# Kernel optimization log

Measured on AMD Instinct MI355X. Metric: run time of the kernel, lower is better.

Reference implementation:

```python
import jax, jax.numpy as jnp
import numpy as np

N = 50000        # nodes
E = 1600000      # edges (before self loops)
D_IN = 768       # roberta-base hidden size
SIZES = [256, 256]
NEG_SLOPE = 0.2
EPS = 1e-16


def setup_inputs() -> dict:
    key = jax.random.key(0)
    ks = jax.random.split(key, 16)
    s = 0.05
    inp = {
        "x": jax.random.normal(ks[0], (N, D_IN), dtype=jnp.float32),
        "edge_index": jax.random.randint(ks[1], (2, E), 0, N, dtype=jnp.int64),
        # GAT layer 0
        "W0": jax.random.normal(ks[2], (D_IN, SIZES[0]), dtype=jnp.float32) * s,
        "a_src0": jax.random.normal(ks[3], (SIZES[0],), dtype=jnp.float32) * s,
        "a_dst0": jax.random.normal(ks[4], (SIZES[0],), dtype=jnp.float32) * s,
        "b0": jnp.zeros((SIZES[0],), dtype=jnp.float32),
        # GAT layer 1
        "W1": jax.random.normal(ks[5], (SIZES[0], SIZES[1]), dtype=jnp.float32) * s,
        "a_src1": jax.random.normal(ks[6], (SIZES[1],), dtype=jnp.float32) * s,
        "a_dst1": jax.random.normal(ks[7], (SIZES[1],), dtype=jnp.float32) * s,
        "b1": jnp.zeros((SIZES[1],), dtype=jnp.float32),
        # GlobalAttention gate_nn: Linear(256 -> 1)
        "gate_w": jax.random.normal(ks[8], (SIZES[1], 1), dtype=jnp.float32) * s,
        "gate_b": jnp.zeros((1,), dtype=jnp.float32),
    }
    return inp


def _gat_layer(x, src, dst, W, a_src, a_dst, b):
    # PyG GATConv, heads=1: h = x W; e_ij = leaky_relu(a_src.h_j + a_dst.h_i)
    # softmax over edges grouped by target node i, then weighted aggregation.
    h = x @ W                                   # [N, D]
    alpha_src = h @ a_src                       # [N]
    alpha_dst = h @ a_dst                       # [N]
    e = jax.nn.leaky_relu(alpha_src[src] + alpha_dst[dst], NEG_SLOPE)  # [E']
    e_max = jax.ops.segment_max(e, dst, num_segments=N)
    e = jnp.exp(e - e_max[dst])
    denom = jax.ops.segment_sum(e, dst, num_segments=N)
    alpha = e / (denom[dst] + EPS)              # [E'] softmax per target
    out = jax.ops.segment_sum(alpha[:, None] * h[src], dst, num_segments=N)
    return out + b


def reference(x, edge_index, W0, a_src0, a_dst0, b0, W1, a_src1, a_dst1, b1, gate_w, gate_b):
    # add self loops (GATConv default add_self_loops=True)
    loop = jnp.arange(N, dtype=edge_index.dtype)
    src = jnp.concatenate([edge_index[0], loop])
    dst = jnp.concatenate([edge_index[1], loop])

    h = jax.nn.relu(_gat_layer(x, src, dst, W0, a_src0, a_dst0, b0))
    h = jax.nn.relu(_gat_layer(h, src, dst, W1, a_src1, a_dst1, b1))

    # GlobalAttention pooling over the single graph
    gate = h @ gate_w + gate_b                  # [N, 1]
    attn = jax.nn.softmax(gate, axis=0)         # softmax over nodes
    out = jnp.sum(attn * h, axis=0, keepdims=True)  # [1, 256]
    return out
```

## Files before the change

kernel.cpp:

```cpp
#include <hip/hip_runtime.h>

typedef unsigned int uint;
typedef unsigned short u16;
typedef unsigned char u8;

typedef __attribute__((ext_vector_type(8))) short short8;
typedef __attribute__((ext_vector_type(8))) u16 u16x8;
typedef __attribute__((ext_vector_type(4))) float f32x4;
typedef __attribute__((ext_vector_type(2))) float f32x2;

#define NN 50000
#define EE 1600000
#define ETOT (EE + NN)
#define NBUCK 782
#define ACHUNK 8192
#define CAP 2432
#define NSLOT 64
#define SLOTW 260

__device__ __forceinline__ u16 f2bf(float f) {
  uint u = __builtin_bit_cast(uint, f);
  uint r = u + 0x7fffu + ((u >> 16) & 1u);
  return (u16)(r >> 16);
}
__device__ __forceinline__ float bf2f(u16 h) {
  return __builtin_bit_cast(float, ((uint)h) << 16);
}
__device__ __forceinline__ u8 f2fp8(float f) {
  int t = __builtin_amdgcn_cvt_pk_fp8_f32(f, f, 0, false);
  return (u8)(t & 0xff);
}
__device__ __forceinline__ float wred_sum(float v) {
#pragma unroll
  for (int off = 32; off > 0; off >>= 1) v += __shfl_xor(v, off);
  return v;
}

__global__ void zero_ws(uint* __restrict__ bnxt, float* __restrict__ slots) {
  int i = blockIdx.x * 256 + threadIdx.x;
  if (i < NBUCK) bnxt[i] = 0u;
  if (i < NSLOT * SLOTW) slots[i] = 0.f;
}

__global__ void wt_both(const float* __restrict__ W0, const float* __restrict__ W1,
                        u16* __restrict__ Wt0, u16* __restrict__ Wt1) {
  int i = blockIdx.x * 256 + threadIdx.x;
  if (i < 768 * 256) {
    int k = i >> 8, n = i & 255;
    Wt0[n * 768 + k] = f2bf(W0[i]);
  } else if (i < 768 * 256 + 256 * 256) {
    int j = i - 768 * 256;
    int k = j >> 8, n = j & 255;
    Wt1[n * 256 + k] = f2bf(W1[j]);
  }
}

template <bool ABF16>
__global__ __launch_bounds__(512) void gemm_fused(const void* __restrict__ Avoid,
                                                  const u16* __restrict__ Bt,
                                                  u8* __restrict__ C8,
                                                  const float* __restrict__ a_src,
                                                  const float* __restrict__ a_dst,
                                                  float* __restrict__ as_,
                                                  float* __restrict__ ad_,
                                                  int M, int K) {
  __shared__ __align__(16) u16 As[128 * 64];
  __shared__ __align__(16) u16 Bs[256 * 64];
  __shared__ float asLds[4][128];
  __shared__ float adLds[4][128];
  const int m0 = blockIdx.x * 128;
  const int tid = threadIdx.x;
  const int lane = tid & 63;
  const int wv = tid >> 6;
  const int wm = wv >> 2, wn = wv & 3;

  f32x4 acc[4][4] = {};

  const int sr = tid >> 2;
  const int skc = (tid & 3) * 16;
  const int br = tid >> 1;
  const int bk = (tid & 1) * 32;

  for (int k0 = 0; k0 < K; k0 += 64) {
    {
      int grow = m0 + sr;
      if constexpr (!ABF16) {
        const float* A = (const float*)Avoid;
        float4 f[4];
        if (grow < M) {
          const float4* src = reinterpret_cast<const float4*>(A + (size_t)grow * K + k0 + skc);
#pragma unroll
          for (int i = 0; i < 4; ++i) f[i] = src[i];
        } else {
#pragma unroll
          for (int i = 0; i < 4; ++i) f[i] = make_float4(0.f, 0.f, 0.f, 0.f);
        }
#pragma unroll
        for (int i = 0; i < 2; ++i) {
          u16x8 v;
          v[0] = f2bf(f[2 * i].x); v[1] = f2bf(f[2 * i].y);
          v[2] = f2bf(f[2 * i].z); v[3] = f2bf(f[2 * i].w);
          v[4] = f2bf(f[2 * i + 1].x); v[5] = f2bf(f[2 * i + 1].y);
          v[6] = f2bf(f[2 * i + 1].z); v[7] = f2bf(f[2 * i + 1].w);
          int k = skc + i * 8;
          int idx = (sr << 6) + (k ^ ((sr & 7) << 3));
          *reinterpret_cast<u16x8*>(&As[idx]) = v;
        }
      } else {
        const u16* A = (const u16*)Avoid;
        u16x8 v[2];
        if (grow < M) {
          const u16x8* src = reinterpret_cast<const u16x8*>(A + (size_t)grow * K + k0 + skc);
          v[0] = src[0]; v[1] = src[1];
        } else {
          v[0] = (u16x8)0; v[1] = (u16x8)0;
        }
#pragma unroll
        for (int i = 0; i < 2; ++i) {
          int k = skc + i * 8;
          int idx = (sr << 6) + (k ^ ((sr & 7) << 3));
          *reinterpret_cast<u16x8*>(&As[idx]) = v[i];
        }
      }
    }
    {
      const u16x8* src = reinterpret_cast<const u16x8*>(Bt + (size_t)br * K + k0 + bk);
#pragma unroll
      for (int i = 0; i < 4; ++i) {
        u16x8 v = src[i];
        int k = bk + i * 8;
        int idx = (br << 6) + (k ^ ((br & 7) << 3));
        *reinterpret_cast<u16x8*>(&Bs[idx]) = v;
      }
    }
    __syncthreads();
#pragma unroll
    for (int kk = 0; kk < 2; ++kk) {
      short8 af[4], bfr[4];
      const int kb = kk * 32 + (lane >> 4) * 8;
#pragma unroll
      for (int m = 0; m < 4; ++m) {
        int r = wm * 64 + m * 16 + (lane & 15);
        int idx = (r << 6) + (kb ^ ((r & 7) << 3));
        af[m] = *reinterpret_cast<const short8*>(&As[idx]);
      }
#pragma unroll
      for (int n = 0; n < 4; ++n) {
        int c = wn * 64 + n * 16 + (lane & 15);
        int idx = (c << 6) + (kb ^ ((c & 7) << 3));
        bfr[n] = *reinterpret_cast<const short8*>(&Bs[idx]);
      }
#pragma unroll
      for (int m = 0; m < 4; ++m)
#pragma unroll
        for (int n = 0; n < 4; ++n)
          acc[m][n] = __builtin_amdgcn_mfma_f32_16x16x32_bf16(af[m], bfr[n], acc[m][n], 0, 0, 0);
    }
    __syncthreads();
  }

  const int g = lane >> 4;
  const int cl = lane & 15;
  float asv[4], adv[4];
#pragma unroll
  for (int n = 0; n < 4; ++n) {
    int c = wn * 64 + n * 16 + cl;
    asv[n] = a_src[c];
    adv[n] = a_dst[c];
  }
#pragma unroll
  for (int m = 0; m < 4; ++m) {
#pragma unroll
    for (int reg = 0; reg < 4; ++reg) {
      int rl = wm * 64 + m * 16 + g * 4 + reg;
      int row = m0 + rl;
      float ps = 0.f, pd = 0.f;
      if (row < M) {
#pragma unroll
        for (int n = 0; n < 4; ++n) {
          float v = acc[m][n][reg];
          C8[(size_t)row * 256 + wn * 64 + n * 16 + cl] = f2fp8(v);
          ps = fmaf(v, asv[n], ps);
          pd = fmaf(v, adv[n], pd);
        }
      }
#pragma unroll
      for (int off = 1; off < 16; off <<= 1) {
        ps += __shfl_xor(ps, off);
        pd += __shfl_xor(pd, off);
      }
      if (cl == 0) {
        asLds[wn][rl] = ps;
        adLds[wn][rl] = pd;
      }
    }
  }
  __syncthreads();
  if (tid < 128) {
    int row = m0 + tid;
    if (row < M) {
      as_[row] = asLds[0][tid] + asLds[1][tid] + asLds[2][tid] + asLds[3][tid];
      ad_[row] = adLds[0][tid] + adLds[1][tid] + adLds[2][tid] + adLds[3][tid];
    }
  }
}

__global__ __launch_bounds__(256) void bucket_scatter(const int* __restrict__ esrc,
                                                      const int* __restrict__ edst,
                                                      uint* __restrict__ bnxt,
                                                      uint* __restrict__ tmp) {
  __shared__ uint lh[NBUCK];
  int base = blockIdx.x * ACHUNK;
  int nE = ETOT - base; if (nE > ACHUNK) nE = ACHUNK;
  for (int i = threadIdx.x; i < NBUCK; i += 256) lh[i] = 0;
  __syncthreads();
  for (int k = threadIdx.x; k < nE; k += 256) {
    int e = base + k;
    int d = (e < EE) ? edst[e] : (e - EE);
    atomicAdd(&lh[d >> 6], 1u);
  }
  __syncthreads();
  for (int i = threadIdx.x; i < NBUCK; i += 256) {
    uint c = lh[i];
    lh[i] = c ? atomicAdd(&bnxt[i], c) : 0u;
  }
  __syncthreads();
  for (int k = threadIdx.x; k < nE; k += 256) {
    int e = base + k;
    int s, d;
    if (e < EE) { s = esrc[e]; d = edst[e]; } else { s = e - EE; d = s; }
    uint pos = atomicAdd(&lh[d >> 6], 1u);
    tmp[(size_t)(d >> 6) * CAP + pos] = ((uint)(d & 63) << 16) | (uint)s;
  }
}

__global__ __launch_bounds__(1024) void scanb_kernel(const uint* __restrict__ bnxt,
                                                     uint* __restrict__ bptr) {
  __shared__ uint wsum[16];
  int tid = threadIdx.x, lane = tid & 63, w = tid >> 6;
  uint v = (tid < NBUCK) ? bnxt[tid] : 0u;
  uint x = v;
#pragma unroll
  for (int off = 1; off < 64; off <<= 1) {
    uint t = __shfl_up(x, off);
    if (lane >= off) x += t;
  }
  if (lane == 63) wsum[w] = x;
  __syncthreads();
  uint woff = 0;
  for (int k = 0; k < w; ++k) woff += wsum[k];
  uint excl = woff + x - v;
  if (tid < NBUCK) bptr[tid] = excl;
}

__global__ __launch_bounds__(256) void bucket_sort(const uint* __restrict__ tmp,
                                                   const uint* __restrict__ bptr,
                                                   const uint* __restrict__ bnxt,
                                                   uint* __restrict__ row_ptr,
                                                   u16* __restrict__ csr) {
  __shared__ uint lh[64];
  __shared__ uint buf[CAP];
  int b = blockIdx.x;
  uint s0 = bptr[b];
  int cnt = (int)bnxt[b];
  int tid = threadIdx.x;
  if (tid < 64) lh[tid] = 0;
  __syncthreads();
  for (int i = tid; i < cnt; i += 256) {
    uint v = tmp[(size_t)b * CAP + i];
    buf[i] = v;
    atomicAdd(&lh[v >> 16], 1u);
  }
  __syncthreads();
  if (tid < 64) {
    uint v = lh[tid];
    uint x = v;
#pragma unroll
    for (int off = 1; off < 64; off <<= 1) {
      uint t = __shfl_up(x, off);
      if (tid >= off) x += t;
    }
    uint pos = s0 + x - v;
    int d = b * 64 + tid;
    if (d < NN) row_ptr[d] = pos;
    lh[tid] = pos;
    if (b == NBUCK - 1 && tid == 0) row_ptr[NN] = s0 + (uint)cnt;
  }
  __syncthreads();
  for (int i = tid; i < cnt; i += 256) {
    uint v = buf[i];
    uint pos = atomicAdd(&lh[v >> 16], 1u);
    csr[pos] = (u16)(v & 0xFFFFu);
  }
}

template <bool POOL>
__global__ __launch_bounds__(256) void agg_kernel(const uint* __restrict__ h8,
                                                  const float* __restrict__ as_,
                                                  const float* __restrict__ ad_,
                                                  const uint* __restrict__ row_ptr,
                                                  const u16* __restrict__ csr_src,
                                                  const float* __restrict__ bias,
                                                  u16* __restrict__ out,
                                                  const float* __restrict__ gate_w,
                                                  float* __restrict__ slots, int n) {
  __shared__ float lp[257];
  int wid = (blockIdx.x * 256 + threadIdx.x) >> 6;
  int lane = threadIdx.x & 63;
  if (POOL) {
    for (int i = threadIdx.x; i < 257; i += 256) lp[i] = 0.f;
    __syncthreads();
  }
  if (wid < n) {
    uint start = row_ptr[wid], end = row_ptr[wid + 1];
    float adi = ad_[wid];
    float ax = 0.f, ay = 0.f, az = 0.f, aw = 0.f;
    float denom = 0.f;
    for (uint base = start; base < end; base += 64) {
      int cnt = (int)(end - base);
      if (cnt > 64) cnt = 64;
      float w = 0.f;
      int s = 0;
      if (lane < cnt) {
        s = (int)csr_src[base + lane];
        float e = as_[s] + adi;
        e = e > 0.f ? e : 0.2f * e;
        w = __expf(e);
      }
      denom += w;
      int j = 0;
      for (; j + 8 <= cnt; j += 8) {
        uint v[8];
        float ww[8];
#pragma unroll
        for (int q = 0; q < 8; ++q) {
          int sq = __shfl(s, j + q);
          ww[q] = __shfl(w, j + q);
          v[q] = h8[(size_t)sq * 64 + lane];
        }
#pragma unroll
        for (int q = 0; q < 8; ++q) {
          f32x2 lo = __builtin_amdgcn_cvt_pk_f32_fp8(v[q], false);
          f32x2 hi = __builtin_amdgcn_cvt_pk_f32_fp8(v[q], true);
          ax = fmaf(ww[q], lo.x, ax); ay = fmaf(ww[q], lo.y, ay);
          az = fmaf(ww[q], hi.x, az); aw = fmaf(ww[q], hi.y, aw);
        }
      }
      for (; j < cnt; ++j) {
        int sj = __shfl(s, j);
        float wj = __shfl(w, j);
        uint v = h8[(size_t)sj * 64 + lane];
        f32x2 lo = __builtin_amdgcn_cvt_pk_f32_fp8(v, false);
        f32x2 hi = __builtin_amdgcn_cvt_pk_f32_fp8(v, true);
        ax = fmaf(wj, lo.x, ax); ay = fmaf(wj, lo.y, ay);
        az = fmaf(wj, hi.x, az); aw = fmaf(wj, hi.y, aw);
      }
    }
    denom = wred_sum(denom);
    float inv = 1.f / (denom + 1e-16f);
    float4 b = reinterpret_cast<const float4*>(bias)[lane];
    float ox = fmaxf(fmaf(ax, inv, b.x), 0.f);
    float oy = fmaxf(fmaf(ay, inv, b.y), 0.f);
    float oz = fmaxf(fmaf(az, inv, b.z), 0.f);
    float ow = fmaxf(fmaf(aw, inv, b.w), 0.f);
    if (!POOL) {
      ushort4 o;
      o.x = f2bf(ox); o.y = f2bf(oy); o.z = f2bf(oz); o.w = f2bf(ow);
      reinterpret_cast<ushort4*>(out)[(size_t)wid * 64 + lane] = o;
    } else {
      float4 gv = reinterpret_cast<const float4*>(gate_w)[lane];
      float pg = wred_sum(ox * gv.x + oy * gv.y + oz * gv.z + ow * gv.w);
      float we = __expf(pg);
      int c0 = lane * 4;
      atomicAdd(&lp[c0 + 0], we * ox);
      atomicAdd(&lp[c0 + 1], we * oy);
      atomicAdd(&lp[c0 + 2], we * oz);
      atomicAdd(&lp[c0 + 3], we * ow);
      if (lane == 0) atomicAdd(&lp[256], we);
    }
  }
  if (POOL) {
    __syncthreads();
    int slot = blockIdx.x & (NSLOT - 1);
    for (int i = threadIdx.x; i < 257; i += 256) {
      float v = lp[i];
      if (v != 0.f) atomicAdd(&slots[slot * SLOTW + i], v);
    }
  }
}

__global__ void pool3_kernel(const float* __restrict__ slots, float* __restrict__ out) {
  __shared__ float dsh;
  int tid = threadIdx.x;
  float acc = 0.f;
  for (int s = 0; s < NSLOT; ++s) acc += slots[s * SLOTW + tid];
  if (tid == 0) {
    float d = 0.f;
    for (int s = 0; s < NSLOT; ++s) d += slots[s * SLOTW + 256];
    dsh = d;
  }
  __syncthreads();
  out[tid] = acc / dsh;
}

extern "C" void kernel_launch(void* const* d_in, const int* in_sizes, int n_in,
                              void* d_out, int out_size, void* d_ws, size_t ws_size,
                              hipStream_t stream) {
  const float* x = (const float*)d_in[0];
  const int* edge = (const int*)d_in[1];
  const float* W0 = (const float*)d_in[2];
  const float* a_src0 = (const float*)d_in[3];
  const float* a_dst0 = (const float*)d_in[4];
  const float* b0 = (const float*)d_in[5];
  const float* W1 = (const float*)d_in[6];
  const float* a_src1 = (const float*)d_in[7];
  const float* a_dst1 = (const float*)d_in[8];
  const float* b1 = (const float*)d_in[9];
  const float* gate_w = (const float*)d_in[10];
  float* out = (float*)d_out;

  char* p = (char*)d_ws;
  size_t off = 0;
  auto take = [&](size_t bytes) -> char* {
    char* r = p + off;
    off = (off + bytes + 255) & ~(size_t)255;
    return r;
  };
  u8* hA = (u8*)take((size_t)NN * 256);
  u16* hB = (u16*)take((size_t)NN * 256 * 2);
  u16* Wt0 = (u16*)take((size_t)256 * 768 * 2);
  u16* Wt1 = (u16*)take((size_t)256 * 256 * 2);
  float* as0 = (float*)take((size_t)NN * 4);
  float* ad0 = (float*)take((size_t)NN * 4);
  float* as1 = (float*)take((size_t)NN * 4);
  float* ad1 = (float*)take((size_t)NN * 4);
  float* slots = (float*)take((size_t)NSLOT * SLOTW * 4);
  uint* bptr = (uint*)take((size_t)NBUCK * 4);
  uint* bnxt = (uint*)take((size_t)NBUCK * 4);
  uint* row_ptr = (uint*)take((size_t)(NN + 1) * 4);
  uint* tmp = (uint*)take((size_t)NBUCK * CAP * 4);
  u16* csr = (u16*)take((size_t)ETOT * 2);

  const int* edge_src = edge;
  const int* edge_dst = edge + EE;

  zero_ws<<<(NSLOT * SLOTW + 255) / 256, 256, 0, stream>>>(bnxt, slots);
  wt_both<<<1024, 256, 0, stream>>>(W0, W1, Wt0, Wt1);

  bucket_scatter<<<(ETOT + ACHUNK - 1) / ACHUNK, 256, 0, stream>>>(edge_src, edge_dst, bnxt, tmp);
  scanb_kernel<<<1, 1024, 0, stream>>>(bnxt, bptr);
  bucket_sort<<<NBUCK, 256, 0, stream>>>(tmp, bptr, bnxt, row_ptr, csr);

  const int ggrid = (NN + 127) / 128;
  gemm_fused<false><<<ggrid, 512, 0, stream>>>(x, Wt0, hA, a_src0, a_dst0, as0, ad0, NN, 768);
  agg_kernel<false><<<12500, 256, 0, stream>>>((const uint*)hA, as0, ad0, row_ptr, csr, b0, hB,
                                               gate_w, slots, NN);
  gemm_fused<true><<<ggrid, 512, 0, stream>>>(hB, Wt1, hA, a_src1, a_dst1, as1, ad1, NN, 256);
  agg_kernel<true><<<12500, 256, 0, stream>>>((const uint*)hA, as1, ad1, row_ptr, csr, b1, nullptr,
                                              gate_w, slots, NN);

  pool3_kernel<<<1, 256, 0, stream>>>(slots, out);
}
```

Baseline: 293.1 us.

## Gather neighbor rows with 16-byte loads across four edge groups per wave

In the aggregation kernel, each wave now splits into four 16-lane groups. Each group handles a different neighbor edge and loads its fp8 row with uint4 (16-byte) loads, so every lane accumulates 16 channels instead of 4. The four partial accumulators are then reduced through shared memory before the normalization, bias, ReLU and pooling steps. This is meant to cut the number of load instructions and raise bytes per request on the random gather. The cost is more registers, an extra LDS transpose/reduction step, and masked work in the edge-count tail.

```diff
diff --git a/kernel.cpp b/kernel.cpp
--- a/kernel.cpp
+++ b/kernel.cpp
@@ -294,8 +294,29 @@
   }
 }
 
+#define FMA16(v, wg)                                                                   \
+  do {                                                                                 \
+    f32x2 p_;                                                                          \
+    p_ = __builtin_amdgcn_cvt_pk_f32_fp8((v).x, false);                                \
+    acc[0] = fmaf((wg), p_.x, acc[0]); acc[1] = fmaf((wg), p_.y, acc[1]);              \
+    p_ = __builtin_amdgcn_cvt_pk_f32_fp8((v).x, true);                                 \
+    acc[2] = fmaf((wg), p_.x, acc[2]); acc[3] = fmaf((wg), p_.y, acc[3]);              \
+    p_ = __builtin_amdgcn_cvt_pk_f32_fp8((v).y, false);                                \
+    acc[4] = fmaf((wg), p_.x, acc[4]); acc[5] = fmaf((wg), p_.y, acc[5]);              \
+    p_ = __builtin_amdgcn_cvt_pk_f32_fp8((v).y, true);                                 \
+    acc[6] = fmaf((wg), p_.x, acc[6]); acc[7] = fmaf((wg), p_.y, acc[7]);              \
+    p_ = __builtin_amdgcn_cvt_pk_f32_fp8((v).z, false);                                \
+    acc[8] = fmaf((wg), p_.x, acc[8]); acc[9] = fmaf((wg), p_.y, acc[9]);              \
+    p_ = __builtin_amdgcn_cvt_pk_f32_fp8((v).z, true);                                 \
+    acc[10] = fmaf((wg), p_.x, acc[10]); acc[11] = fmaf((wg), p_.y, acc[11]);          \
+    p_ = __builtin_amdgcn_cvt_pk_f32_fp8((v).w, false);                                \
+    acc[12] = fmaf((wg), p_.x, acc[12]); acc[13] = fmaf((wg), p_.y, acc[13]);          \
+    p_ = __builtin_amdgcn_cvt_pk_f32_fp8((v).w, true);                                 \
+    acc[14] = fmaf((wg), p_.x, acc[14]); acc[15] = fmaf((wg), p_.y, acc[15]);          \
+  } while (0)
+
 template <bool POOL>
-__global__ __launch_bounds__(256) void agg_kernel(const uint* __restrict__ h8,
+__global__ __launch_bounds__(256) void agg_kernel(const uint4* __restrict__ h16,
                                                   const float* __restrict__ as_,
                                                   const float* __restrict__ ad_,
                                                   const uint* __restrict__ row_ptr,
@@ -304,9 +325,12 @@
                                                   u16* __restrict__ out,
                                                   const float* __restrict__ gate_w,
                                                   float* __restrict__ slots, int n) {
+  __shared__ float tr[4][4][16][16];
   __shared__ float lp[257];
-  int wid = (blockIdx.x * 256 + threadIdx.x) >> 6;
+  int wv = threadIdx.x >> 6;
+  int wid = blockIdx.x * 4 + wv;
   int lane = threadIdx.x & 63;
+  int g = lane >> 4, li = lane & 15;
   if (POOL) {
     for (int i = threadIdx.x; i < 257; i += 256) lp[i] = 0.f;
     __syncthreads();
@@ -314,7 +338,9 @@
   if (wid < n) {
     uint start = row_ptr[wid], end = row_ptr[wid + 1];
     float adi = ad_[wid];
-    float ax = 0.f, ay = 0.f, az = 0.f, aw = 0.f;
+    float acc[16];
+#pragma unroll
+    for (int c = 0; c < 16; ++c) acc[c] = 0.f;
     float denom = 0.f;
     for (uint base = start; base < end; base += 64) {
       int cnt = (int)(end - base);
@@ -330,33 +356,37 @@
       denom += w;
       int j = 0;
       for (; j + 8 <= cnt; j += 8) {
-        uint v[8];
-        float ww[8];
-#pragma unroll
-        for (int q = 0; q < 8; ++q) {
-          int sq = __shfl(s, j + q);
-          ww[q] = __shfl(w, j + q);
-          v[q] = h8[(size_t)sq * 64 + lane];
-        }
-#pragma unroll
-        for (int q = 0; q < 8; ++q) {
-          f32x2 lo = __builtin_amdgcn_cvt_pk_f32_fp8(v[q], false);
-          f32x2 hi = __builtin_amdgcn_cvt_pk_f32_fp8(v[q], true);
-          ax = fmaf(ww[q], lo.x, ax); ay = fmaf(ww[q], lo.y, ay);
-          az = fmaf(ww[q], hi.x, az); aw = fmaf(ww[q], hi.y, aw);
-        }
-      }
-      for (; j < cnt; ++j) {
-        int sj = __shfl(s, j);
-        float wj = __shfl(w, j);
-        uint v = h8[(size_t)sj * 64 + lane];
-        f32x2 lo = __builtin_amdgcn_cvt_pk_f32_fp8(v, false);
-        f32x2 hi = __builtin_amdgcn_cvt_pk_f32_fp8(v, true);
-        ax = fmaf(wj, lo.x, ax); ay = fmaf(wj, lo.y, ay);
-        az = fmaf(wj, hi.x, az); aw = fmaf(wj, hi.y, aw);
+        int s0 = __shfl(s, j + g);
+        int s1 = __shfl(s, j + 4 + g);
+        float w0 = __shfl(w, j + g);
+        float w1 = __shfl(w, j + 4 + g);
+        uint4 v0 = h16[(size_t)s0 * 16 + li];
+        uint4 v1 = h16[(size_t)s1 * 16 + li];
+        FMA16(v0, w0);
+        FMA16(v1, w1);
+      }
+      for (; j < cnt; j += 4) {
+        int jg = j + g;
+        int sg = __shfl(s, jg & 63);
+        float wg = __shfl(w, jg & 63);
+        if (jg >= cnt) wg = 0.f;
+        uint4 v = h16[(size_t)sg * 16 + li];
+        FMA16(v, wg);
       }
     }
     denom = wred_sum(denom);
+    *reinterpret_cast<float4*>(&tr[wv][g][li][0])  = make_float4(acc[0], acc[1], acc[2], acc[3]);
+    *reinterpret_cast<float4*>(&tr[wv][g][li][4])  = make_float4(acc[4], acc[5], acc[6], acc[7]);
+    *reinterpret_cast<float4*>(&tr[wv][g][li][8])  = make_float4(acc[8], acc[9], acc[10], acc[11]);
+    *reinterpret_cast<float4*>(&tr[wv][g][li][12]) = make_float4(acc[12], acc[13], acc[14], acc[15]);
+    asm volatile("s_waitcnt lgkmcnt(0)" ::: "memory");
+    __builtin_amdgcn_sched_barrier(0);
+    float ax = 0.f, ay = 0.f, az = 0.f, aw = 0.f;
+#pragma unroll
+    for (int gg = 0; gg < 4; ++gg) {
+      float4 rv = *reinterpret_cast<const float4*>(&tr[wv][gg][lane >> 2][4 * (lane & 3)]);
+      ax += rv.x; ay += rv.y; az += rv.z; aw += rv.w;
+    }
     float inv = 1.f / (denom + 1e-16f);
     float4 b = reinterpret_cast<const float4*>(bias)[lane];
     float ox = fmaxf(fmaf(ax, inv, b.x), 0.f);
@@ -453,10 +483,10 @@
 
   const int ggrid = (NN + 127) / 128;
   gemm_fused<false><<<ggrid, 512, 0, stream>>>(x, Wt0, hA, a_src0, a_dst0, as0, ad0, NN, 768);
-  agg_kernel<false><<<12500, 256, 0, stream>>>((const uint*)hA, as0, ad0, row_ptr, csr, b0, hB,
+  agg_kernel<false><<<12500, 256, 0, stream>>>((const uint4*)hA, as0, ad0, row_ptr, csr, b0, hB,
                                                gate_w, slots, NN);
   gemm_fused<true><<<ggrid, 512, 0, stream>>>(hB, Wt1, hA, a_src1, a_dst1, as1, ad1, NN, 256);
-  agg_kernel<true><<<12500, 256, 0, stream>>>((const uint*)hA, as1, ad1, row_ptr, csr, b1, nullptr,
+  agg_kernel<true><<<12500, 256, 0, stream>>>((const uint4*)hA, as1, ad1, row_ptr, csr, b1, nullptr,
                                               gate_w, slots, NN);
 
   pool3_kernel<<<1, 256, 0, stream>>>(slots, out);
```

Result: faster. 282.9 us (-3.5%).
